# Optimization experiments

Hardware: AMD Instinct MI355X
Metric: run time of the kernel (lower is better)

Reference implementation:

```python
import jax, jax.numpy as jnp
import numpy as np

B, S, H, A = 16, 2048, 512, 256


def setup_inputs() -> dict:
    key = jax.random.key(0)
    k1, k2, k3 = jax.random.split(key, 3)
    x = jax.random.normal(k1, (B, S, H), dtype=jnp.float32)
    W_a = jax.random.normal(k2, (A, H), dtype=jnp.float32) * (1.0 / np.sqrt(H))
    q = jax.random.normal(k3, (1, A), dtype=jnp.float32) * (1.0 / np.sqrt(A))
    return {"x": x, "W_a": W_a, "q": q}


def reference(x, W_a, q):
    # x: [B,S,H], W_a: [A,H], q: [1,A]
    Bm, Sm, Hm = x.shape
    # Per-key score e[b,t] = q . tanh(W_a @ x[b,t]).
    # In the original, keys for t > s are zeroed BEFORE the bias-free linear;
    # tanh(0)=0 and the -inf softmax mask removes those entries, so the score
    # is independent of the query position s -> no O(S^2*H*A) recompute needed.
    e = jnp.einsum('oa,bta->bt', q, jnp.tanh(jnp.einsum('bth,ah->bta', x, W_a)))  # [B,S]
    causal = jnp.where(jnp.tril(jnp.ones((Sm, Sm), dtype=bool)), 0.0, -jnp.inf)  # [S_query, S_key]
    logits = e[:, None, :] + causal[None, :, :]            # [B,S,S]
    d = jax.nn.softmax(logits, axis=-1)                    # attention over keys t<=s
    # masked values v_masked[b,s,t,:] = [t<=s]*x[b,t,:]; d is already 0 for t>s
    a = jnp.einsum('bst,bth->bsh', d, x)                   # [B,S,H]
    return a[:, :, None, :], d[:, :, None, :]              # [B,S,1,H], [B,S,1,S] as in torch
```

## Files before the change

kernel.cpp:

```cpp
#include <hip/hip_runtime.h>
#include <hip/hip_bf16.h>
#include <math.h>

#define BB 16
#define SS 2048
#define HH 512
#define AA 256
#define NCH 128
#define CT  (SS/NCH)
#define XST 72

typedef short bf16x8 __attribute__((ext_vector_type(8)));
typedef float f32x4  __attribute__((ext_vector_type(4)));

__device__ __forceinline__ short f2bf(float f) {
    union { __hip_bfloat16 h; short s; } u;
    u.h = __float2bfloat16(f);
    return u.s;
}

__device__ __forceinline__ void nt_store4(float4 v, float4* p) {
    f32x4 o = {v.x, v.y, v.z, v.w};
    __builtin_nontemporal_store(o, (f32x4*)p);
}

__global__ __launch_bounds__(256) void convW_kernel(
    const float* __restrict__ W, short* __restrict__ Wb)
{
    int i = blockIdx.x * 256 + threadIdx.x;
    float4 v = ((const float4*)W)[i];
    short4 o = make_short4(f2bf(v.x), f2bf(v.y), f2bf(v.z), f2bf(v.w));
    ((short4*)Wb)[i] = o;
}

__global__ __launch_bounds__(256, 2) void gemm_e_mfma(
    const float* __restrict__ x, const short* __restrict__ Wb,
    const float* __restrict__ q, float* __restrict__ e)
{
    __shared__ short Xl[64 * XST];
    __shared__ short Wl[256 * XST];
    __shared__ float epart[2][64];

    const int tid  = threadIdx.x;
    const int lane = tid & 63;
    const int wv   = tid >> 6;
    const int wm   = wv & 1;
    const int wn   = wv >> 1;
    const int quad = lane >> 4;
    const int col  = lane & 15;
    const long tok0 = (long)blockIdx.x * 64;

    f32x4 acc[2][8];
    #pragma unroll
    for (int mt = 0; mt < 2; mt++)
        #pragma unroll
        for (int nt = 0; nt < 8; nt++) acc[mt][nt] = (f32x4){0.f, 0.f, 0.f, 0.f};

    for (int kc = 0; kc < HH; kc += 64) {
        __syncthreads();
        #pragma unroll
        for (int i = 0; i < 2; i++) {
            int task = i * 256 + tid;
            int row = task >> 3, seg = task & 7;
            const float* src = &x[(tok0 + row) * HH + kc + seg * 8];
            float4 v0 = *(const float4*)src;
            float4 v1 = *(const float4*)(src + 4);
            bf16x8 o;
            o[0] = f2bf(v0.x); o[1] = f2bf(v0.y); o[2] = f2bf(v0.z); o[3] = f2bf(v0.w);
            o[4] = f2bf(v1.x); o[5] = f2bf(v1.y); o[6] = f2bf(v1.z); o[7] = f2bf(v1.w);
            *(bf16x8*)&Xl[row * XST + seg * 8] = o;
        }
        #pragma unroll
        for (int i = 0; i < 8; i++) {
            int task = i * 256 + tid;
            int row = task >> 3, seg = task & 7;
            bf16x8 v = *(const bf16x8*)&Wb[row * HH + kc + seg * 8];
            *(bf16x8*)&Wl[row * XST + seg * 8] = v;
        }
        __syncthreads();
        #pragma unroll
        for (int kk = 0; kk < 64; kk += 32) {
            bf16x8 af[2], bfr[8];
            #pragma unroll
            for (int mt = 0; mt < 2; mt++)
                af[mt] = *(bf16x8*)&Xl[(wm * 32 + mt * 16 + col) * XST + kk + quad * 8];
            #pragma unroll
            for (int nt = 0; nt < 8; nt++)
                bfr[nt] = *(bf16x8*)&Wl[(wn * 128 + nt * 16 + col) * XST + kk + quad * 8];
            #pragma unroll
            for (int mt = 0; mt < 2; mt++)
                #pragma unroll
                for (int nt = 0; nt < 8; nt++)
                    acc[mt][nt] = __builtin_amdgcn_mfma_f32_16x16x32_bf16(
                        af[mt], bfr[nt], acc[mt][nt], 0, 0, 0);
        }
    }

    float qv[8];
    #pragma unroll
    for (int nt = 0; nt < 8; nt++) qv[nt] = q[wn * 128 + nt * 16 + col];
    #pragma unroll
    for (int mt = 0; mt < 2; mt++) {
        #pragma unroll
        for (int reg = 0; reg < 4; reg++) {
            float sv = 0.f;
            #pragma unroll
            for (int nt = 0; nt < 8; nt++) sv += qv[nt] * tanhf(acc[mt][nt][reg]);
            #pragma unroll
            for (int off = 1; off < 16; off <<= 1) sv += __shfl_xor(sv, off, 64);
            if (col == 0)
                epart[wn][wm * 32 + mt * 16 + quad * 4 + reg] = sv;
        }
    }
    __syncthreads();
    if (tid < 64) e[tok0 + tid] = epart[0][tid] + epart[1][tid];
}

__global__ __launch_bounds__(256) void softmax_scan_kernel(
    const float* __restrict__ e, float* __restrict__ w, float* __restrict__ zinv)
{
    __shared__ float red[256];
    const int b = blockIdx.x, tid = threadIdx.x;
    const float* eb = e + b * SS;
    float v[8];
    #pragma unroll
    for (int j = 0; j < 8; j++) v[j] = eb[tid * 8 + j];
    float m = v[0];
    #pragma unroll
    for (int j = 1; j < 8; j++) m = fmaxf(m, v[j]);
    red[tid] = m; __syncthreads();
    for (int st = 128; st > 0; st >>= 1) {
        if (tid < st) red[tid] = fmaxf(red[tid], red[tid + st]);
        __syncthreads();
    }
    const float mb = red[0];
    __syncthreads();
    float we[8], pf[8], p = 0.f;
    #pragma unroll
    for (int j = 0; j < 8; j++) { we[j] = expf(v[j] - mb); p += we[j]; pf[j] = p; }
    red[tid] = p; __syncthreads();
    for (int st = 1; st < 256; st <<= 1) {
        float t = (tid >= st) ? red[tid - st] : 0.f;
        __syncthreads();
        red[tid] += t;
        __syncthreads();
    }
    const float excl = red[tid] - p;
    #pragma unroll
    for (int j = 0; j < 8; j++) {
        float Z = excl + pf[j];
        w[b * SS + tid * 8 + j]    = we[j];
        zinv[b * SS + tid * 8 + j] = 1.0f / Z;
    }
}

__global__ __launch_bounds__(256) void write_d_kernel(
    const float* __restrict__ w, const float* __restrict__ zinv,
    float* __restrict__ dout)
{
    const int bs = blockIdx.x;
    const int b  = bs >> 11;
    const int s  = bs & (SS - 1);
    const float zi = zinv[bs];
    const float4* wb = (const float4*)(w + b * SS);
    float4* row = (float4*)(dout + (size_t)bs * SS);
    #pragma unroll
    for (int r = 0; r < 2; r++) {
        int t4 = r * 256 + threadIdx.x;
        int t  = t4 * 4;
        float4 wv = wb[t4];
        float4 o;
        o.x = (t + 0 <= s) ? wv.x * zi : 0.f;
        o.y = (t + 1 <= s) ? wv.y * zi : 0.f;
        o.z = (t + 2 <= s) ? wv.z * zi : 0.f;
        o.w = (t + 3 <= s) ? wv.w * zi : 0.f;
        nt_store4(o, &row[t4]);
    }
}

__global__ __launch_bounds__(128) void scan_part_kernel(
    const float* __restrict__ x, const float* __restrict__ w, float* __restrict__ P)
{
    const int blk = blockIdx.x;
    const int b = blk >> 7;
    const int c = blk & (NCH - 1);
    const int tid = threadIdx.x;
    const int t0 = c * CT;
    const float4* xb = (const float4*)(x + ((size_t)b * SS + t0) * HH);
    const float* wb = w + b * SS + t0;
    float4 acc = make_float4(0.f, 0.f, 0.f, 0.f);
    #pragma unroll 4
    for (int t = 0; t < CT; t++) {
        float wt = wb[t];
        float4 xv = xb[(size_t)t * (HH / 4) + tid];
        acc.x = fmaf(wt, xv.x, acc.x);
        acc.y = fmaf(wt, xv.y, acc.y);
        acc.z = fmaf(wt, xv.z, acc.z);
        acc.w = fmaf(wt, xv.w, acc.w);
    }
    ((float4*)P)[(size_t)blk * (HH / 4) + tid] = acc;
}

__global__ __launch_bounds__(128) void chunk_prefix_kernel(float* __restrict__ P)
{
    const int b = blockIdx.x, tid = threadIdx.x;
    float4* Pb = (float4*)P + (size_t)b * NCH * (HH / 4) + tid;
    float4 run = make_float4(0.f, 0.f, 0.f, 0.f);
    for (int c = 0; c < NCH; c += 4) {
        float4 p0 = Pb[(size_t)(c + 0) * (HH / 4)];
        float4 p1 = Pb[(size_t)(c + 1) * (HH / 4)];
        float4 p2 = Pb[(size_t)(c + 2) * (HH / 4)];
        float4 p3 = Pb[(size_t)(c + 3) * (HH / 4)];
        Pb[(size_t)(c + 0) * (HH / 4)] = run;
        run.x += p0.x; run.y += p0.y; run.z += p0.z; run.w += p0.w;
        Pb[(size_t)(c + 1) * (HH / 4)] = run;
        run.x += p1.x; run.y += p1.y; run.z += p1.z; run.w += p1.w;
        Pb[(size_t)(c + 2) * (HH / 4)] = run;
        run.x += p2.x; run.y += p2.y; run.z += p2.z; run.w += p2.w;
        Pb[(size_t)(c + 3) * (HH / 4)] = run;
        run.x += p3.x; run.y += p3.y; run.z += p3.z; run.w += p3.w;
    }
}

__global__ __launch_bounds__(128) void scan_emit_kernel(
    const float* __restrict__ x, const float* __restrict__ w,
    const float* __restrict__ zinv, const float* __restrict__ P,
    float* __restrict__ aout)
{
    const int blk = blockIdx.x;
    const int b = blk >> 7;
    const int c = blk & (NCH - 1);
    const int tid = threadIdx.x;
    float4 base = ((const float4*)P)[(size_t)blk * (HH / 4) + tid];
    const int t0 = c * CT;
    const float4* xb = (const float4*)(x + ((size_t)b * SS + t0) * HH);
    const float* wb = w + b * SS + t0;
    const float* zb = zinv + b * SS + t0;
    float4* ab = (float4*)(aout + ((size_t)b * SS + t0) * HH);
    #pragma unroll 4
    for (int t = 0; t < CT; t++) {
        float wt = wb[t];
        float zi = zb[t];
        float4 xv = xb[(size_t)t * (HH / 4) + tid];
        base.x = fmaf(wt, xv.x, base.x);
        base.y = fmaf(wt, xv.y, base.y);
        base.z = fmaf(wt, xv.z, base.z);
        base.w = fmaf(wt, xv.w, base.w);
        float4 o = make_float4(base.x * zi, base.y * zi, base.z * zi, base.w * zi);
        nt_store4(o, &ab[(size_t)t * (HH / 4) + tid]);
    }
}

extern "C" void kernel_launch(void* const* d_in, const int* in_sizes, int n_in,
                              void* d_out, int out_size, void* d_ws, size_t ws_size,
                              hipStream_t stream)
{
    const float* x = (const float*)d_in[0];
    const float* W = (const float*)d_in[1];
    const float* q = (const float*)d_in[2];
    float* out  = (float*)d_out;
    float* aout = out;
    float* dout = out + (size_t)BB * SS * HH;

    float* ws   = (float*)d_ws;
    float* e    = ws;
    float* w    = ws + BB * SS;
    float* zinv = ws + 2 * BB * SS;
    float* P    = ws + 3 * BB * SS;
    short* Wb   = (short*)(ws + 3 * BB * SS + BB * NCH * HH);

    hipLaunchKernelGGL(convW_kernel, dim3(AA * HH / 4 / 256), dim3(256), 0, stream,
                       W, Wb);
    hipLaunchKernelGGL(gemm_e_mfma, dim3(BB * SS / 64), dim3(256), 0, stream,
                       x, Wb, q, e);
    hipLaunchKernelGGL(softmax_scan_kernel, dim3(BB), dim3(256), 0, stream,
                       e, w, zinv);
    hipLaunchKernelGGL(write_d_kernel, dim3(BB * SS), dim3(256), 0, stream,
                       w, zinv, dout);
    hipLaunchKernelGGL(scan_part_kernel, dim3(BB * NCH), dim3(128), 0, stream,
                       x, w, P);
    hipLaunchKernelGGL(chunk_prefix_kernel, dim3(BB), dim3(128), 0, stream,
                       P);
    hipLaunchKernelGGL(scan_emit_kernel, dim3(BB * NCH), dim3(128), 0, stream,
                       x, w, zinv, P, aout);
}
```

Baseline: 432.6 us.

## Drop chunk prefix kernel, batch d-row writes, use wave-shuffle softmax scan

Removes the separate chunk_prefix launch: each scan_emit block now sums the earlier chunk partials itself, with the chunk count halved to keep that redundant prefix work small. write_d_kernel now writes 16 rows per block and reuses the loaded w vector across them, cutting block count and repeated loads. The softmax block reduction and scan switch from shared-memory tree loops with many barriers to wave shuffles. The trade-off is fewer, larger scan blocks (less parallelism) and a redundant O(NCH) prefix read per block.

```diff
diff --git a/kernel.cpp b/kernel.cpp
--- a/kernel.cpp
+++ b/kernel.cpp
@@ -6,7 +6,7 @@
 #define SS 2048
 #define HH 512
 #define AA 256
-#define NCH 128
+#define NCH 64
 #define CT  (SS/NCH)
 #define XST 72
 
@@ -119,8 +119,10 @@
 __global__ __launch_bounds__(256) void softmax_scan_kernel(
     const float* __restrict__ e, float* __restrict__ w, float* __restrict__ zinv)
 {
-    __shared__ float red[256];
+    __shared__ float wmax[4];
+    __shared__ float wsum[4];
     const int b = blockIdx.x, tid = threadIdx.x;
+    const int lane = tid & 63, wvi = tid >> 6;
     const float* eb = e + b * SS;
     float v[8];
     #pragma unroll
@@ -128,24 +130,25 @@
     float m = v[0];
     #pragma unroll
     for (int j = 1; j < 8; j++) m = fmaxf(m, v[j]);
-    red[tid] = m; __syncthreads();
-    for (int st = 128; st > 0; st >>= 1) {
-        if (tid < st) red[tid] = fmaxf(red[tid], red[tid + st]);
-        __syncthreads();
-    }
-    const float mb = red[0];
+    #pragma unroll
+    for (int off = 32; off > 0; off >>= 1) m = fmaxf(m, __shfl_xor(m, off, 64));
+    if (lane == 0) wmax[wvi] = m;
     __syncthreads();
+    const float mb = fmaxf(fmaxf(wmax[0], wmax[1]), fmaxf(wmax[2], wmax[3]));
     float we[8], pf[8], p = 0.f;
     #pragma unroll
     for (int j = 0; j < 8; j++) { we[j] = expf(v[j] - mb); p += we[j]; pf[j] = p; }
-    red[tid] = p; __syncthreads();
-    for (int st = 1; st < 256; st <<= 1) {
-        float t = (tid >= st) ? red[tid - st] : 0.f;
-        __syncthreads();
-        red[tid] += t;
-        __syncthreads();
-    }
-    const float excl = red[tid] - p;
+    float incl = p;
+    #pragma unroll
+    for (int off = 1; off < 64; off <<= 1) {
+        float t = __shfl_up(incl, off, 64);
+        if (lane >= off) incl += t;
+    }
+    if (lane == 63) wsum[wvi] = incl;
+    __syncthreads();
+    float base = 0.f;
+    for (int ww = 0; ww < wvi; ww++) base += wsum[ww];
+    const float excl = base + incl - p;
     #pragma unroll
     for (int j = 0; j < 8; j++) {
         float Z = excl + pf[j];
@@ -158,23 +161,33 @@
     const float* __restrict__ w, const float* __restrict__ zinv,
     float* __restrict__ dout)
 {
-    const int bs = blockIdx.x;
-    const int b  = bs >> 11;
-    const int s  = bs & (SS - 1);
-    const float zi = zinv[bs];
+    const int blk = blockIdx.x;
+    const int b  = blk >> 7;
+    const int sg = blk & 127;
+    const int s0 = sg << 4;
+    const int tid = threadIdx.x;
     const float4* wb = (const float4*)(w + b * SS);
-    float4* row = (float4*)(dout + (size_t)bs * SS);
-    #pragma unroll
-    for (int r = 0; r < 2; r++) {
-        int t4 = r * 256 + threadIdx.x;
-        int t  = t4 * 4;
-        float4 wv = wb[t4];
-        float4 o;
-        o.x = (t + 0 <= s) ? wv.x * zi : 0.f;
-        o.y = (t + 1 <= s) ? wv.y * zi : 0.f;
-        o.z = (t + 2 <= s) ? wv.z * zi : 0.f;
-        o.w = (t + 3 <= s) ? wv.w * zi : 0.f;
-        nt_store4(o, &row[t4]);
+    const float4 wa = wb[tid];
+    const float4 wc = wb[tid + 256];
+    const int ta = tid * 4;
+    const int tc = (tid + 256) * 4;
+    const float* zb = zinv + b * SS + s0;
+    float4* rowbase = (float4*)(dout + (size_t)(b * SS + s0) * SS);
+    #pragma unroll
+    for (int r = 0; r < 16; r++) {
+        const int s = s0 + r;
+        const float zi = zb[r];
+        float4 oa, oc;
+        oa.x = (ta + 0 <= s) ? wa.x * zi : 0.f;
+        oa.y = (ta + 1 <= s) ? wa.y * zi : 0.f;
+        oa.z = (ta + 2 <= s) ? wa.z * zi : 0.f;
+        oa.w = (ta + 3 <= s) ? wa.w * zi : 0.f;
+        oc.x = (tc + 0 <= s) ? wc.x * zi : 0.f;
+        oc.y = (tc + 1 <= s) ? wc.y * zi : 0.f;
+        oc.z = (tc + 2 <= s) ? wc.z * zi : 0.f;
+        oc.w = (tc + 3 <= s) ? wc.w * zi : 0.f;
+        nt_store4(oa, rowbase + (size_t)r * (SS / 4) + tid);
+        nt_store4(oc, rowbase + (size_t)r * (SS / 4) + tid + 256);
     }
 }
 
@@ -182,7 +195,7 @@
     const float* __restrict__ x, const float* __restrict__ w, float* __restrict__ P)
 {
     const int blk = blockIdx.x;
-    const int b = blk >> 7;
+    const int b = blk >> 6;
     const int c = blk & (NCH - 1);
     const int tid = threadIdx.x;
     const int t0 = c * CT;
@@ -201,37 +214,21 @@
     ((float4*)P)[(size_t)blk * (HH / 4) + tid] = acc;
 }
 
-__global__ __launch_bounds__(128) void chunk_prefix_kernel(float* __restrict__ P)
-{
-    const int b = blockIdx.x, tid = threadIdx.x;
-    float4* Pb = (float4*)P + (size_t)b * NCH * (HH / 4) + tid;
-    float4 run = make_float4(0.f, 0.f, 0.f, 0.f);
-    for (int c = 0; c < NCH; c += 4) {
-        float4 p0 = Pb[(size_t)(c + 0) * (HH / 4)];
-        float4 p1 = Pb[(size_t)(c + 1) * (HH / 4)];
-        float4 p2 = Pb[(size_t)(c + 2) * (HH / 4)];
-        float4 p3 = Pb[(size_t)(c + 3) * (HH / 4)];
-        Pb[(size_t)(c + 0) * (HH / 4)] = run;
-        run.x += p0.x; run.y += p0.y; run.z += p0.z; run.w += p0.w;
-        Pb[(size_t)(c + 1) * (HH / 4)] = run;
-        run.x += p1.x; run.y += p1.y; run.z += p1.z; run.w += p1.w;
-        Pb[(size_t)(c + 2) * (HH / 4)] = run;
-        run.x += p2.x; run.y += p2.y; run.z += p2.z; run.w += p2.w;
-        Pb[(size_t)(c + 3) * (HH / 4)] = run;
-        run.x += p3.x; run.y += p3.y; run.z += p3.z; run.w += p3.w;
-    }
-}
-
 __global__ __launch_bounds__(128) void scan_emit_kernel(
     const float* __restrict__ x, const float* __restrict__ w,
     const float* __restrict__ zinv, const float* __restrict__ P,
     float* __restrict__ aout)
 {
     const int blk = blockIdx.x;
-    const int b = blk >> 7;
+    const int b = blk >> 6;
     const int c = blk & (NCH - 1);
     const int tid = threadIdx.x;
-    float4 base = ((const float4*)P)[(size_t)blk * (HH / 4) + tid];
+    const float4* Pb = (const float4*)P + (size_t)b * NCH * (HH / 4) + tid;
+    float4 base = make_float4(0.f, 0.f, 0.f, 0.f);
+    for (int cc = 0; cc < c; cc++) {
+        float4 p = Pb[(size_t)cc * (HH / 4)];
+        base.x += p.x; base.y += p.y; base.z += p.z; base.w += p.w;
+    }
     const int t0 = c * CT;
     const float4* xb = (const float4*)(x + ((size_t)b * SS + t0) * HH);
     const float* wb = w + b * SS + t0;
@@ -275,12 +272,10 @@
                        x, Wb, q, e);
     hipLaunchKernelGGL(softmax_scan_kernel, dim3(BB), dim3(256), 0, stream,
                        e, w, zinv);
-    hipLaunchKernelGGL(write_d_kernel, dim3(BB * SS), dim3(256), 0, stream,
+    hipLaunchKernelGGL(write_d_kernel, dim3(BB * SS / 16), dim3(256), 0, stream,
                        w, zinv, dout);
     hipLaunchKernelGGL(scan_part_kernel, dim3(BB * NCH), dim3(128), 0, stream,
                        x, w, P);
-    hipLaunchKernelGGL(chunk_prefix_kernel, dim3(BB), dim3(128), 0, stream,
-                       P);
     hipLaunchKernelGGL(scan_emit_kernel, dim3(BB * NCH), dim3(128), 0, stream,
                        x, w, zinv, P, aout);
 }
```

Result: no change. 436.3 us (+0.9%).
